# Kernel tuning notes

Measured on AMD Instinct MI355X. Metric: run time of the kernel, lower is better.

The kernel has to match this reference:

```python
import jax, jax.numpy as jnp
import numpy as np

B, C, H, W = 8, 256, 64, 64
D = C // 8  # query/key channels


def setup_inputs() -> dict:
    key = jax.random.key(0)
    ks = jax.random.split(key, 7)
    s = 0.05
    x = jax.random.normal(ks[0], (B, C, H, W), dtype=jnp.float32)
    Wq = jax.random.normal(ks[1], (D, C), dtype=jnp.float32) * s
    bq = jax.random.normal(ks[2], (D,), dtype=jnp.float32) * s
    Wk = jax.random.normal(ks[3], (D, C), dtype=jnp.float32) * s
    bk = jax.random.normal(ks[4], (D,), dtype=jnp.float32) * s
    Wv = jax.random.normal(ks[5], (C, C), dtype=jnp.float32) * s
    bv = jax.random.normal(ks[6], (C,), dtype=jnp.float32) * s
    return {"x": x, "Wq": Wq, "bq": bq, "Wk": Wk, "bk": bk, "Wv": Wv, "bv": bv}


def reference(x, Wq, bq, Wk, bk, Wv, bv):
    b, c, h, w = x.shape
    n = h * w
    xf = x.reshape(b, c, n)  # (B, C, HW)
    # 1x1 convs == per-pixel linear projections
    q = jnp.einsum('dc,bcn->bdn', Wq, xf) + bq[None, :, None]  # (B, D, HW)
    k = jnp.einsum('dc,bcn->bdn', Wk, xf) + bk[None, :, None]  # (B, D, HW)
    v = jnp.einsum('ec,bcn->ben', Wv, xf) + bv[None, :, None]  # (B, C, HW)
    # attention[b, n, m] = sum_d q[b,d,n] * k[b,d,m]  (no 1/sqrt(d) scaling)
    attn = jax.nn.softmax(jnp.einsum('bdn,bdm->bnm', q, k), axis=-1)
    # out[b,c,n] = sum_m v[b,c,m] * attn[b,n,m]  (v @ attn^T)
    out = jnp.einsum('bcm,bnm->bcn', v, attn)
    return out.reshape(b, c, h, w) + x
```

## Files before the change

kernel.cpp:

```cpp
#include <hip/hip_runtime.h>
#include <stdint.h>

#define BN 4096
#define NCH 256
#define DQ 32

typedef _Float16 half8  __attribute__((ext_vector_type(8)));
typedef _Float16 half4  __attribute__((ext_vector_type(4)));
typedef _Float16 half2  __attribute__((ext_vector_type(2)));
typedef float   floatx4  __attribute__((ext_vector_type(4)));
typedef float   floatx16 __attribute__((ext_vector_type(16)));

typedef __attribute__((address_space(1))) const void g1_void;
typedef __attribute__((address_space(3))) void l3_void;

#define LOG2E 1.44269504088896f
#define EXP2F(x) __builtin_amdgcn_exp2f(x)
#define LOG2F(x) __builtin_amdgcn_logf(x)

__global__ __launch_bounds__(256) void convert_w(
    const float* __restrict__ Wq, const float* __restrict__ Wk,
    const float* __restrict__ Wv, _Float16* __restrict__ W16)
{
    int e4 = (blockIdx.x * 256 + threadIdx.x) * 4;
    float4 v;
    if (e4 < 8192)        v = *(const float4*)&Wq[e4];
    else if (e4 < 16384) {
        v = *(const float4*)&Wk[e4 - 8192];
        v.x *= LOG2E; v.y *= LOG2E; v.z *= LOG2E; v.w *= LOG2E;
    }
    else                  v = *(const float4*)&Wv[e4 - 16384];
    half4 h = { (_Float16)v.x, (_Float16)v.y, (_Float16)v.z, (_Float16)v.w };
    *(half4*)&W16[e4] = h;
}

__global__ __launch_bounds__(512) void proj_kernel(
    const float* __restrict__ x, const _Float16* __restrict__ W16,
    const float* __restrict__ bq, const float* __restrict__ bk,
    const float* __restrict__ bv,
    _Float16* __restrict__ qT, _Float16* __restrict__ kT,
    _Float16* __restrict__ vb)
{
    const int t  = threadIdx.x;
    const int n0 = blockIdx.x * 128;
    const int b  = blockIdx.z;

    __shared__ __align__(16) _Float16 xTl[128 * 256];

#pragma unroll
    for (int p = 0; p < 2; ++p) {
        const int kb = p * 128 + (t >> 5) * 8;
        const int n4 = (t & 31) * 4;
        float4 xr[8];
#pragma unroll
        for (int i = 0; i < 8; ++i)
            xr[i] = *(const float4*)&x[((size_t)b * NCH + kb + i) * BN + n0 + n4];
        const float* xf = (const float*)xr;
#pragma unroll
        for (int j = 0; j < 4; ++j) {
            const int n = n4 + j;
            half8 hv;
#pragma unroll
            for (int i = 0; i < 8; ++i) hv[i] = (_Float16)xf[i * 4 + j];
            const int phys = (kb >> 3) ^ ((n >> 2) & 31);
            *(half8*)&xTl[n * 256 + phys * 8] = hv;
        }
    }
    __syncthreads();

    const int lane  = t & 63;
    const int gw    = blockIdx.y * 8 + (t >> 6);
    const int col32 = lane & 31;
    const int h     = lane >> 5;
    const int nc    = gw & 3;
    const int jj    = gw >> 2;

    const _Float16* Wq16 = W16;
    const _Float16* Wk16 = W16 + 8192;
    const _Float16* Wv16 = W16 + 16384;

#define XFRAG(ks) (*(const half8*)&xTl[(nc * 32 + col32) * 256 + \
        (((ks) * 2 + h) ^ (((nc * 32 + col32) >> 2) & 31)) * 8])

    if (jj == 0) {
        const float bqv = bq[col32];
        const float bkv = bk[col32] * LOG2E;
        floatx16 aq, ak2;
#pragma unroll
        for (int r = 0; r < 16; ++r) { aq[r] = 0.0f; ak2[r] = 0.0f; }
#pragma unroll
        for (int ks = 0; ks < 16; ++ks) {
            half8 xa = XFRAG(ks);
            half8 wqf = *(const half8*)&Wq16[col32 * 256 + ks * 16 + h * 8];
            half8 wkf = *(const half8*)&Wk16[col32 * 256 + ks * 16 + h * 8];
            aq  = __builtin_amdgcn_mfma_f32_32x32x16_f16(xa, wqf, aq, 0, 0, 0);
            ak2 = __builtin_amdgcn_mfma_f32_32x32x16_f16(xa, wkf, ak2, 0, 0, 0);
        }
#pragma unroll
        for (int r = 0; r < 16; ++r) {
            const int n = n0 + nc * 32 + (r & 3) + 8 * (r >> 2) + 4 * h;
            qT[((size_t)b * BN + n) * DQ + col32] = (_Float16)(aq[r] + bqv);
            kT[((size_t)b * BN + n) * DQ + col32] = (_Float16)(ak2[r] + bkv);
        }
    } else {
        const int rg_lo = (jj == 1) ? 0 : (jj == 2) ? 3 : 6;
        const int rg_hi = (jj == 1) ? 3 : (jj == 2) ? 6 : 8;
        for (int rg = rg_lo; rg < rg_hi; ++rg) {
            floatx16 av;
#pragma unroll
            for (int r = 0; r < 16; ++r) av[r] = 0.0f;
#pragma unroll
            for (int ks = 0; ks < 16; ++ks) {
                half8 xb  = XFRAG(ks);
                half8 wvf = *(const half8*)&Wv16[(rg * 32 + col32) * 256 + ks * 16 + h * 8];
                av = __builtin_amdgcn_mfma_f32_32x32x16_f16(wvf, xb, av, 0, 0, 0);
            }
#pragma unroll
            for (int r = 0; r < 16; ++r) {
                const int c = rg * 32 + (r & 3) + 8 * (r >> 2) + 4 * h;
                vb[((size_t)b * NCH + c) * BN + n0 + nc * 32 + col32] =
                    (_Float16)(av[r] + bv[c]);
            }
        }
    }
#undef XFRAG
}

__global__ __launch_bounds__(256, 3) void flash_kernel(
    const _Float16* __restrict__ qT, const _Float16* __restrict__ kT,
    const _Float16* __restrict__ vb,
    _Float16* __restrict__ Op, float* __restrict__ Ml, int KPS)
{
    const int t    = threadIdx.x;
    const int lane = t & 63;
    const int w    = t >> 6;
    const int n0   = blockIdx.x * 64;
    const int kh   = blockIdx.y;
    const int b    = blockIdx.z;
    const int kbase = kh * KPS;
    const int iters = (min(KPS, BN - kbase)) >> 6;

    __shared__ __align__(16) _Float16 vs[NCH * 64];
    __shared__ __align__(16) _Float16 Ps[2][64 * 64];
    __shared__ float alph_s[2][64];
    __shared__ float l_s[64];

    const int col   = lane & 15;
    const int q4    = lane >> 4;
    const int col32 = lane & 31;
    const int h     = lane >> 5;

    const _Float16* kp = kT + (size_t)b * BN * DQ;
    const _Float16* vp = vb + (size_t)b * NCH * BN;

    half8 bqf = *(const half8*)&qT[((size_t)b * BN + n0 + w * 16 + col) * DQ + q4 * 8];

    floatx16 acc[2][2];
#pragma unroll
    for (int ct = 0; ct < 2; ++ct)
#pragma unroll
        for (int nt = 0; nt < 2; ++nt)
#pragma unroll
            for (int r = 0; r < 16; ++r) acc[ct][nt][r] = 0.0f;

    float m_i = -1e30f, l_i = 0.0f;

    const int sc_loc = lane >> 3;
    const int s_log  = (lane & 7) ^ (sc_loc & 7);

    half8 ak[4];
    floatx4 sf[4];
    half4 pk[4];
    float al;

#define K_LOAD(MC)                                                          \
    do {                                                                    \
        _Pragma("unroll")                                                   \
        for (int mt = 0; mt < 4; ++mt)                                      \
            ak[mt] = *(const half8*)&kp[(size_t)((MC) + mt * 16 + col) * DQ + q4 * 8]; \
    } while (0)

#define V_DMA(MC)                                                           \
    do {                                                                    \
        _Pragma("unroll")                                                   \
        for (int j = 0; j < 8; ++j) {                                       \
            const int c = w * 64 + j * 8 + sc_loc;                          \
            __builtin_amdgcn_global_load_lds(                               \
                (g1_void*)&vp[(size_t)c * BN + (MC) + s_log * 8],           \
                (l3_void*)&vs[(w * 64 + j * 8) * 64], 16, 0, 0);            \
        }                                                                   \
    } while (0)

#define QK_STEP()                                                           \
    do {                                                                    \
        __builtin_amdgcn_s_setprio(1);                                      \
        _Pragma("unroll")                                                   \
        for (int mt = 0; mt < 4; ++mt) {                                    \
            floatx4 z = { 0.0f, 0.0f, 0.0f, 0.0f };                         \
            sf[mt] = __builtin_amdgcn_mfma_f32_16x16x32_f16(ak[mt], bqf, z, 0, 0, 0); \
        }                                                                   \
        __builtin_amdgcn_s_setprio(0);                                      \
    } while (0)

#define SM_STEP()                                                           \
    do {                                                                    \
        float cmax = -1e30f;                                                \
        _Pragma("unroll")                                                   \
        for (int mt = 0; mt < 4; ++mt)                                      \
            _Pragma("unroll")                                               \
            for (int r = 0; r < 4; ++r) cmax = fmaxf(cmax, sf[mt][r]);      \
        cmax = fmaxf(cmax, __shfl_xor(cmax, 16));                           \
        cmax = fmaxf(cmax, __shfl_xor(cmax, 32));                           \
        const float mn = (cmax > m_i + 8.0f) ? cmax : m_i;                  \
        al = EXP2F(m_i - mn);                                               \
        float csum = 0.0f;                                                  \
        _Pragma("unroll")                                                   \
        for (int mt = 0; mt < 4; ++mt) {                                    \
            float p0 = EXP2F(sf[mt][0] - mn);                               \
            float p1 = EXP2F(sf[mt][1] - mn);                               \
            float p2 = EXP2F(sf[mt][2] - mn);                               \
            float p3 = EXP2F(sf[mt][3] - mn);                               \
            csum += p0 + p1 + p2 + p3;                                      \
            half2 q01 = __builtin_bit_cast(half2, __builtin_amdgcn_cvt_pkrtz(p0, p1)); \
            half2 q23 = __builtin_bit_cast(half2, __builtin_amdgcn_cvt_pkrtz(p2, p3)); \
            pk[mt][0] = q01[0]; pk[mt][1] = q01[1];                         \
            pk[mt][2] = q23[0]; pk[mt][3] = q23[1];                         \
        }                                                                   \
        csum += __shfl_xor(csum, 16);                                       \
        csum += __shfl_xor(csum, 32);                                       \
        l_i = l_i * al + csum;                                              \
        m_i = mn;                                                           \
    } while (0)

#define PS_WRITE(BUF)                                                       \
    do {                                                                    \
        const int n = w * 16 + col;                                         \
        _Pragma("unroll")                                                   \
        for (int mt = 0; mt < 4; ++mt) {                                    \
            const int p_log = 2 * mt + (q4 >> 1);                           \
            const int p_phys = p_log ^ (n & 7);                             \
            *(half4*)((char*)&Ps[BUF][n * 64] + p_phys * 16 + (q4 & 1) * 8) = pk[mt]; \
        }                                                                   \
        if (q4 == 0) alph_s[BUF][n] = al;                                   \
    } while (0)

#define RESCALE(BUF)                                                        \
    do {                                                                    \
        float a0 = alph_s[BUF][col32];                                      \
        float a1 = alph_s[BUF][32 + col32];                                 \
        if (!__all((a0 == 1.0f) && (a1 == 1.0f))) {                         \
            _Pragma("unroll")                                               \
            for (int ct = 0; ct < 2; ++ct)                                  \
                _Pragma("unroll")                                           \
                for (int r = 0; r < 16; ++r) {                              \
                    acc[ct][0][r] *= a0;                                    \
                    acc[ct][1][r] *= a1;                                    \
                }                                                           \
        }                                                                   \
    } while (0)

#define PV_STEP(BUF)                                                        \
    do {                                                                    \
        __builtin_amdgcn_s_setprio(1);                                      \
        _Pragma("unroll")                                                   \
        for (int ks = 0; ks < 4; ++ks) {                                    \
            const int p_log = 2 * ks + h;                                   \
            half8 bp0 = *(const half8*)((char*)&Ps[BUF][col32 * 64] + (p_log ^ (col32 & 7)) * 16); \
            half8 bp1 = *(const half8*)((char*)&Ps[BUF][(32 + col32) * 64] + (p_log ^ (col32 & 7)) * 16); \
            _Pragma("unroll")                                               \
            for (int ct = 0; ct < 2; ++ct) {                                \
                const int c = w * 64 + ct * 32 + col32;                     \
                half8 av = *(const half8*)((char*)&vs[c * 64] + ((p_log ^ (c & 7)) * 16)); \
                acc[ct][0] = __builtin_amdgcn_mfma_f32_32x32x16_f16(av, bp0, acc[ct][0], 0, 0, 0); \
                acc[ct][1] = __builtin_amdgcn_mfma_f32_32x32x16_f16(av, bp1, acc[ct][1], 0, 0, 0); \
            }                                                               \
        }                                                                   \
        __builtin_amdgcn_s_setprio(0);                                      \
    } while (0)

    K_LOAD(kbase);
    V_DMA(kbase);
    QK_STEP();
    { const int m1 = (1 < iters) ? kbase + 64 : kbase; K_LOAD(m1); }
    SM_STEP();
    PS_WRITE(0);

    for (int it = 0; it < iters - 1; ++it) {
        const int cur = it & 1, nxt = cur ^ 1;
        asm volatile("s_waitcnt lgkmcnt(0)" ::: "memory");
        __builtin_amdgcn_s_barrier();
        QK_STEP();
        { const int m2 = (it + 2 < iters) ? kbase + (it + 2) * 64
                                          : kbase + (iters - 1) * 64;
          K_LOAD(m2); }
        RESCALE(cur);
        asm volatile("s_waitcnt vmcnt(4)" ::: "memory");
        PV_STEP(cur);
        SM_STEP();
        PS_WRITE(nxt);
        asm volatile("s_waitcnt lgkmcnt(0)" ::: "memory");
        V_DMA(kbase + (it + 1) * 64);
    }

    {
        const int cur = (iters - 1) & 1;
        asm volatile("s_waitcnt lgkmcnt(0)" ::: "memory");
        __builtin_amdgcn_s_barrier();
        RESCALE(cur);
        asm volatile("s_waitcnt vmcnt(0)" ::: "memory");
        PV_STEP(cur);
    }

    if (q4 == 0) {
        const int n = w * 16 + col;
        l_s[n] = l_i;
        Ml[(size_t)(kh * 8 + b) * BN + n0 + n] = m_i + LOG2F(l_i);
    }
    __syncthreads();
    const float li0 = 1.0f / l_s[col32];
    const float li1 = 1.0f / l_s[32 + col32];

    _Float16* Opp = Op + (size_t)(kh * 8 + b) * NCH * BN;
#pragma unroll
    for (int ct = 0; ct < 2; ++ct)
#pragma unroll
        for (int nt = 0; nt < 2; ++nt) {
            const float li = nt ? li1 : li0;
#pragma unroll
            for (int r = 0; r < 16; ++r) {
                int row = (r & 3) + 8 * (r >> 2) + 4 * h;
                int c = w * 64 + ct * 32 + row;
                Opp[(size_t)c * BN + n0 + nt * 32 + col32] = (_Float16)(acc[ct][nt][r] * li);
            }
        }
#undef K_LOAD
#undef V_DMA
#undef QK_STEP
#undef SM_STEP
#undef PS_WRITE
#undef RESCALE
#undef PV_STEP
}

__global__ __launch_bounds__(256) void combine_kernel(
    const _Float16* __restrict__ Op, const float* __restrict__ Ml,
    const float* __restrict__ x, float* __restrict__ out, int nsplit)
{
    const int n  = (blockIdx.x * 256 + threadIdx.x) * 8;
    const int c0 = blockIdx.y * 2;
    const int b  = blockIdx.z;

    float f[3][8];
    float Z[8];
#pragma unroll
    for (int j = 0; j < 8; ++j) Z[j] = -1e30f;
    for (int s = 0; s < nsplit; ++s) {
        const float* mlp = &Ml[(size_t)(s * 8 + b) * BN + n];
        floatx4 z0 = *(const floatx4*)mlp;
        floatx4 z1 = *(const floatx4*)(mlp + 4);
#pragma unroll
        for (int j = 0; j < 4; ++j) { f[s][j] = z0[j]; f[s][4 + j] = z1[j]; }
#pragma unroll
        for (int j = 0; j < 8; ++j) Z[j] = fmaxf(Z[j], f[s][j]);
    }
    float lsum[8];
#pragma unroll
    for (int j = 0; j < 8; ++j) lsum[j] = 0.0f;
    for (int s = 0; s < nsplit; ++s)
#pragma unroll
        for (int j = 0; j < 8; ++j) { f[s][j] = EXP2F(f[s][j] - Z[j]); lsum[j] += f[s][j]; }
#pragma unroll
    for (int j = 0; j < 8; ++j) lsum[j] = 1.0f / lsum[j];
    for (int s = 0; s < nsplit; ++s)
#pragma unroll
        for (int j = 0; j < 8; ++j) f[s][j] *= lsum[j];

#pragma unroll 2
    for (int ci = 0; ci < 2; ++ci) {
        const int c = c0 + ci;
        const size_t off = ((size_t)b * NCH + c) * BN + n;
        const size_t po = (size_t)c * BN + n;
        float ov[8];
#pragma unroll
        for (int j = 0; j < 8; ++j) ov[j] = 0.0f;
        for (int s = 0; s < nsplit; ++s) {
            half8 hv = *(const half8*)&Op[(size_t)(s * 8 + b) * NCH * BN + po];
#pragma unroll
            for (int j = 0; j < 8; ++j) ov[j] += (float)hv[j] * f[s][j];
        }
        floatx4 x0 = *(const floatx4*)&x[off];
        floatx4 x1 = *(const floatx4*)&x[off + 4];
        floatx4 o0, o1;
#pragma unroll
        for (int j = 0; j < 4; ++j) { o0[j] = ov[j] + x0[j]; o1[j] = ov[4 + j] + x1[j]; }
        *(floatx4*)&out[off] = o0;
        *(floatx4*)&out[off + 4] = o1;
    }
}

extern "C" void kernel_launch(void* const* d_in, const int* in_sizes, int n_in,
                              void* d_out, int out_size, void* d_ws, size_t ws_size,
                              hipStream_t stream)
{
    const float* x  = (const float*)d_in[0];
    const float* Wq = (const float*)d_in[1];
    const float* bq = (const float*)d_in[2];
    const float* Wk = (const float*)d_in[3];
    const float* bk = (const float*)d_in[4];
    const float* Wv = (const float*)d_in[5];
    const float* bv = (const float*)d_in[6];
    float* out = (float*)d_out;

    _Float16* ws = (_Float16*)d_ws;
    _Float16* W16 = ws;
    _Float16* qT  = W16 + 81920;
    _Float16* kT  = qT + (size_t)8 * BN * DQ;
    _Float16* vb  = kT + (size_t)8 * BN * DQ;
    _Float16* Op  = vb + (size_t)8 * NCH * BN;

    const size_t baseElems = 81920 + (size_t)2 * 8 * BN * DQ + (size_t)8 * NCH * BN;
    const size_t opElems3  = (size_t)3 * 8 * NCH * BN;
    const size_t mlBytes   = (size_t)24 * BN * sizeof(float);
    const size_t need3     = (baseElems + opElems3) * 2 + mlBytes + 256;
    const int nsplit = (ws_size >= need3) ? 3 : 2;
    const int KPS    = (nsplit == 3) ? 1408 : 2048;

    float* Ml = (float*)(Op + (size_t)nsplit * 8 * NCH * BN);

    convert_w<<<dim3(80), 256, 0, stream>>>(Wq, Wk, Wv, W16);
    proj_kernel<<<dim3(32, 2, 8), 512, 0, stream>>>(x, W16, bq, bk, bv, qT, kT, vb);
    flash_kernel<<<dim3(64, nsplit, 8), 256, 0, stream>>>(qT, kT, vb, Op, Ml, KPS);
    combine_kernel<<<dim3(2, 128, 8), 256, 0, stream>>>(Op, Ml, x, out, nsplit);
}
```

Before: 238.5 us.

## Warp-specialize flash kernel into QK/softmax producer and PV consumer waves

The flash attention block grows to 512 threads. Four waves now compute QK^T and the online softmax and write P and the rescale factors into double-buffered shared memory. The other four waves stream V into LDS and run the PV MFMAs with the accumulators, and the two groups stay in step through a shared barrier each iteration. The goal is to overlap the softmax work with the PV matrix work across waves. The cost is that V load latency is no longer hidden behind the K loads within a wave, and launch bounds of (512, 4) tighten the register budget per wave, which risks spills of the 64-float accumulator.

```diff
diff --git a/kernel.cpp b/kernel.cpp
--- a/kernel.cpp
+++ b/kernel.cpp
@@ -126,14 +126,14 @@
 #undef XFRAG
 }
 
-__global__ __launch_bounds__(256, 3) void flash_kernel(
+__global__ __launch_bounds__(512, 4) void flash_kernel(
     const _Float16* __restrict__ qT, const _Float16* __restrict__ kT,
     const _Float16* __restrict__ vb,
     _Float16* __restrict__ Op, float* __restrict__ Ml, int KPS)
 {
     const int t    = threadIdx.x;
     const int lane = t & 63;
-    const int w    = t >> 6;
+    const int wid  = t >> 6;
     const int n0   = blockIdx.x * 64;
     const int kh   = blockIdx.y;
     const int b    = blockIdx.z;
@@ -150,196 +150,194 @@
     const int col32 = lane & 31;
     const int h     = lane >> 5;
 
-    const _Float16* kp = kT + (size_t)b * BN * DQ;
-    const _Float16* vp = vb + (size_t)b * NCH * BN;
-
-    half8 bqf = *(const half8*)&qT[((size_t)b * BN + n0 + w * 16 + col) * DQ + q4 * 8];
-
-    floatx16 acc[2][2];
-#pragma unroll
-    for (int ct = 0; ct < 2; ++ct)
-#pragma unroll
-        for (int nt = 0; nt < 2; ++nt)
-#pragma unroll
-            for (int r = 0; r < 16; ++r) acc[ct][nt][r] = 0.0f;
-
-    float m_i = -1e30f, l_i = 0.0f;
-
-    const int sc_loc = lane >> 3;
-    const int s_log  = (lane & 7) ^ (sc_loc & 7);
-
-    half8 ak[4];
-    floatx4 sf[4];
-    half4 pk[4];
-    float al;
+    if (wid < 4) {
+        const int w = wid;
+        const _Float16* kp = kT + (size_t)b * BN * DQ;
+
+        half8 bqf = *(const half8*)&qT[((size_t)b * BN + n0 + w * 16 + col) * DQ + q4 * 8];
+        half8 ak[4];
+        floatx4 sf[4];
+        half4 pk[4];
+        float m_i = -1e30f, l_i = 0.0f, al = 1.0f;
 
 #define K_LOAD(MC)                                                          \
-    do {                                                                    \
-        _Pragma("unroll")                                                   \
-        for (int mt = 0; mt < 4; ++mt)                                      \
-            ak[mt] = *(const half8*)&kp[(size_t)((MC) + mt * 16 + col) * DQ + q4 * 8]; \
-    } while (0)
-
-#define V_DMA(MC)                                                           \
-    do {                                                                    \
-        _Pragma("unroll")                                                   \
-        for (int j = 0; j < 8; ++j) {                                       \
-            const int c = w * 64 + j * 8 + sc_loc;                          \
-            __builtin_amdgcn_global_load_lds(                               \
-                (g1_void*)&vp[(size_t)c * BN + (MC) + s_log * 8],           \
-                (l3_void*)&vs[(w * 64 + j * 8) * 64], 16, 0, 0);            \
-        }                                                                   \
-    } while (0)
+        do {                                                                \
+            _Pragma("unroll")                                               \
+            for (int mt = 0; mt < 4; ++mt)                                  \
+                ak[mt] = *(const half8*)&kp[(size_t)((MC) + mt * 16 + col) * DQ + q4 * 8]; \
+        } while (0)
 
 #define QK_STEP()                                                           \
-    do {                                                                    \
-        __builtin_amdgcn_s_setprio(1);                                      \
-        _Pragma("unroll")                                                   \
-        for (int mt = 0; mt < 4; ++mt) {                                    \
-            floatx4 z = { 0.0f, 0.0f, 0.0f, 0.0f };                         \
-            sf[mt] = __builtin_amdgcn_mfma_f32_16x16x32_f16(ak[mt], bqf, z, 0, 0, 0); \
-        }                                                                   \
-        __builtin_amdgcn_s_setprio(0);                                      \
-    } while (0)
+        do {                                                                \
+            __builtin_amdgcn_s_setprio(1);                                  \
+            _Pragma("unroll")                                               \
+            for (int mt = 0; mt < 4; ++mt) {                                \
+                floatx4 z = { 0.0f, 0.0f, 0.0f, 0.0f };                     \
+                sf[mt] = __builtin_amdgcn_mfma_f32_16x16x32_f16(ak[mt], bqf, z, 0, 0, 0); \
+            }                                                               \
+            __builtin_amdgcn_s_setprio(0);                                  \
+        } while (0)
 
 #define SM_STEP()                                                           \
-    do {                                                                    \
-        float cmax = -1e30f;                                                \
-        _Pragma("unroll")                                                   \
-        for (int mt = 0; mt < 4; ++mt)                                      \
-            _Pragma("unroll")                                               \
-            for (int r = 0; r < 4; ++r) cmax = fmaxf(cmax, sf[mt][r]);      \
-        cmax = fmaxf(cmax, __shfl_xor(cmax, 16));                           \
-        cmax = fmaxf(cmax, __shfl_xor(cmax, 32));                           \
-        const float mn = (cmax > m_i + 8.0f) ? cmax : m_i;                  \
-        al = EXP2F(m_i - mn);                                               \
-        float csum = 0.0f;                                                  \
-        _Pragma("unroll")                                                   \
-        for (int mt = 0; mt < 4; ++mt) {                                    \
-            float p0 = EXP2F(sf[mt][0] - mn);                               \
-            float p1 = EXP2F(sf[mt][1] - mn);                               \
-            float p2 = EXP2F(sf[mt][2] - mn);                               \
-            float p3 = EXP2F(sf[mt][3] - mn);                               \
-            csum += p0 + p1 + p2 + p3;                                      \
-            half2 q01 = __builtin_bit_cast(half2, __builtin_amdgcn_cvt_pkrtz(p0, p1)); \
-            half2 q23 = __builtin_bit_cast(half2, __builtin_amdgcn_cvt_pkrtz(p2, p3)); \
-            pk[mt][0] = q01[0]; pk[mt][1] = q01[1];                         \
-            pk[mt][2] = q23[0]; pk[mt][3] = q23[1];                         \
-        }                                                                   \
-        csum += __shfl_xor(csum, 16);                                       \
-        csum += __shfl_xor(csum, 32);                                       \
-        l_i = l_i * al + csum;                                              \
-        m_i = mn;                                                           \
-    } while (0)
+        do {                                                                \
+            float cmax = -1e30f;                                            \
+            _Pragma("unroll")                                               \
+            for (int mt = 0; mt < 4; ++mt)                                  \
+                _Pragma("unroll")                                           \
+                for (int r = 0; r < 4; ++r) cmax = fmaxf(cmax, sf[mt][r]);  \
+            cmax = fmaxf(cmax, __shfl_xor(cmax, 16));                       \
+            cmax = fmaxf(cmax, __shfl_xor(cmax, 32));                       \
+            const float mn = (cmax > m_i + 8.0f) ? cmax : m_i;              \
+            al = EXP2F(m_i - mn);                                           \
+            float csum = 0.0f;                                              \
+            _Pragma("unroll")                                               \
+            for (int mt = 0; mt < 4; ++mt) {                                \
+                float p0 = EXP2F(sf[mt][0] - mn);                           \
+                float p1 = EXP2F(sf[mt][1] - mn);                           \
+                float p2 = EXP2F(sf[mt][2] - mn);                           \
+                float p3 = EXP2F(sf[mt][3] - mn);                           \
+                csum += p0 + p1 + p2 + p3;                                  \
+                half2 q01 = __builtin_bit_cast(half2, __builtin_amdgcn_cvt_pkrtz(p0, p1)); \
+                half2 q23 = __builtin_bit_cast(half2, __builtin_amdgcn_cvt_pkrtz(p2, p3)); \
+                pk[mt][0] = q01[0]; pk[mt][1] = q01[1];                     \
+                pk[mt][2] = q23[0]; pk[mt][3] = q23[1];                     \
+            }                                                               \
+            csum += __shfl_xor(csum, 16);                                   \
+            csum += __shfl_xor(csum, 32);                                   \
+            l_i = l_i * al + csum;                                          \
+            m_i = mn;                                                       \
+        } while (0)
 
 #define PS_WRITE(BUF)                                                       \
-    do {                                                                    \
-        const int n = w * 16 + col;                                         \
-        _Pragma("unroll")                                                   \
-        for (int mt = 0; mt < 4; ++mt) {                                    \
-            const int p_log = 2 * mt + (q4 >> 1);                           \
-            const int p_phys = p_log ^ (n & 7);                             \
-            *(half4*)((char*)&Ps[BUF][n * 64] + p_phys * 16 + (q4 & 1) * 8) = pk[mt]; \
-        }                                                                   \
-        if (q4 == 0) alph_s[BUF][n] = al;                                   \
-    } while (0)
-
-#define RESCALE(BUF)                                                        \
-    do {                                                                    \
-        float a0 = alph_s[BUF][col32];                                      \
-        float a1 = alph_s[BUF][32 + col32];                                 \
-        if (!__all((a0 == 1.0f) && (a1 == 1.0f))) {                         \
-            _Pragma("unroll")                                               \
-            for (int ct = 0; ct < 2; ++ct)                                  \
-                _Pragma("unroll")                                           \
-                for (int r = 0; r < 16; ++r) {                              \
-                    acc[ct][0][r] *= a0;                                    \
-                    acc[ct][1][r] *= a1;                                    \
-                }                                                           \
-        }                                                                   \
-    } while (0)
-
-#define PV_STEP(BUF)                                                        \
-    do {                                                                    \
-        __builtin_amdgcn_s_setprio(1);                                      \
-        _Pragma("unroll")                                                   \
-        for (int ks = 0; ks < 4; ++ks) {                                    \
-            const int p_log = 2 * ks + h;                                   \
-            half8 bp0 = *(const half8*)((char*)&Ps[BUF][col32 * 64] + (p_log ^ (col32 & 7)) * 16); \
-            half8 bp1 = *(const half8*)((char*)&Ps[BUF][(32 + col32) * 64] + (p_log ^ (col32 & 7)) * 16); \
-            _Pragma("unroll")                                               \
-            for (int ct = 0; ct < 2; ++ct) {                                \
-                const int c = w * 64 + ct * 32 + col32;                     \
-                half8 av = *(const half8*)((char*)&vs[c * 64] + ((p_log ^ (c & 7)) * 16)); \
-                acc[ct][0] = __builtin_amdgcn_mfma_f32_32x32x16_f16(av, bp0, acc[ct][0], 0, 0, 0); \
-                acc[ct][1] = __builtin_amdgcn_mfma_f32_32x32x16_f16(av, bp1, acc[ct][1], 0, 0, 0); \
+        do {                                                                \
+            const int n = w * 16 + col;                                     \
+            _Pragma("unroll")                                               \
+            for (int mt = 0; mt < 4; ++mt) {                                \
+                const int p_log = 2 * mt + (q4 >> 1);                       \
+                const int p_phys = p_log ^ (n & 7);                         \
+                *(half4*)((char*)&Ps[BUF][n * 64] + p_phys * 16 + (q4 & 1) * 8) = pk[mt]; \
             }                                                               \
-        }                                                                   \
-        __builtin_amdgcn_s_setprio(0);                                      \
-    } while (0)
-
-    K_LOAD(kbase);
-    V_DMA(kbase);
-    QK_STEP();
-    { const int m1 = (1 < iters) ? kbase + 64 : kbase; K_LOAD(m1); }
-    SM_STEP();
-    PS_WRITE(0);
-
-    for (int it = 0; it < iters - 1; ++it) {
-        const int cur = it & 1, nxt = cur ^ 1;
-        asm volatile("s_waitcnt lgkmcnt(0)" ::: "memory");
-        __builtin_amdgcn_s_barrier();
+            if (q4 == 0) alph_s[BUF][n] = al;                               \
+        } while (0)
+
+        K_LOAD(kbase);
         QK_STEP();
-        { const int m2 = (it + 2 < iters) ? kbase + (it + 2) * 64
-                                          : kbase + (iters - 1) * 64;
-          K_LOAD(m2); }
-        RESCALE(cur);
-        asm volatile("s_waitcnt vmcnt(4)" ::: "memory");
-        PV_STEP(cur);
+        { const int m1 = (1 < iters) ? kbase + 64 : kbase; K_LOAD(m1); }
         SM_STEP();
-        PS_WRITE(nxt);
-        asm volatile("s_waitcnt lgkmcnt(0)" ::: "memory");
-        V_DMA(kbase + (it + 1) * 64);
-    }
-
-    {
-        const int cur = (iters - 1) & 1;
-        asm volatile("s_waitcnt lgkmcnt(0)" ::: "memory");
-        __builtin_amdgcn_s_barrier();
-        RESCALE(cur);
-        asm volatile("s_waitcnt vmcnt(0)" ::: "memory");
-        PV_STEP(cur);
-    }
-
-    if (q4 == 0) {
-        const int n = w * 16 + col;
-        l_s[n] = l_i;
-        Ml[(size_t)(kh * 8 + b) * BN + n0 + n] = m_i + LOG2F(l_i);
-    }
-    __syncthreads();
-    const float li0 = 1.0f / l_s[col32];
-    const float li1 = 1.0f / l_s[32 + col32];
-
-    _Float16* Opp = Op + (size_t)(kh * 8 + b) * NCH * BN;
-#pragma unroll
-    for (int ct = 0; ct < 2; ++ct)
-#pragma unroll
-        for (int nt = 0; nt < 2; ++nt) {
-            const float li = nt ? li1 : li0;
-#pragma unroll
-            for (int r = 0; r < 16; ++r) {
-                int row = (r & 3) + 8 * (r >> 2) + 4 * h;
-                int c = w * 64 + ct * 32 + row;
-                Opp[(size_t)c * BN + n0 + nt * 32 + col32] = (_Float16)(acc[ct][nt][r] * li);
-            }
+        PS_WRITE(0);
+
+        for (int it = 0; it < iters; ++it) {
+            asm volatile("s_waitcnt lgkmcnt(0)" ::: "memory");
+            __builtin_amdgcn_s_barrier();
+            if (it + 1 < iters) {
+                QK_STEP();
+                { const int m2 = (it + 2 < iters) ? kbase + (it + 2) * 64
+                                                  : kbase + (iters - 1) * 64;
+                  K_LOAD(m2); }
+                SM_STEP();
+                PS_WRITE((it + 1) & 1);
+            }
+        }
+
+        if (q4 == 0) {
+            const int n = w * 16 + col;
+            l_s[n] = l_i;
+            Ml[(size_t)(kh * 8 + b) * BN + n0 + n] = m_i + LOG2F(l_i);
         }
 #undef K_LOAD
-#undef V_DMA
 #undef QK_STEP
 #undef SM_STEP
 #undef PS_WRITE
-#undef RESCALE
-#undef PV_STEP
+    } else {
+        const int w = wid - 4;
+        const _Float16* vp = vb + (size_t)b * NCH * BN;
+        const int sc_loc = lane >> 3;
+        const int s_log  = (lane & 7) ^ (sc_loc & 7);
+
+        floatx16 acc[2][2];
+#pragma unroll
+        for (int ct = 0; ct < 2; ++ct)
+#pragma unroll
+            for (int nt = 0; nt < 2; ++nt)
+#pragma unroll
+                for (int r = 0; r < 16; ++r) acc[ct][nt][r] = 0.0f;
+
+#define V_DMA(MC)                                                           \
+        do {                                                                \
+            _Pragma("unroll")                                               \
+            for (int j = 0; j < 8; ++j) {                                   \
+                const int c = w * 64 + j * 8 + sc_loc;                      \
+                __builtin_amdgcn_global_load_lds(                           \
+                    (g1_void*)&vp[(size_t)c * BN + (MC) + s_log * 8],       \
+                    (l3_void*)&vs[(w * 64 + j * 8) * 64], 16, 0, 0);        \
+            }                                                               \
+        } while (0)
+
+        V_DMA(kbase);
+
+        for (int it = 0; it < iters; ++it) {
+            const int cur = it & 1;
+            asm volatile("s_waitcnt lgkmcnt(0)" ::: "memory");
+            __builtin_amdgcn_s_barrier();
+
+            {
+                float a0 = alph_s[cur][col32];
+                float a1 = alph_s[cur][32 + col32];
+                if (!__all((a0 == 1.0f) && (a1 == 1.0f))) {
+#pragma unroll
+                    for (int ct = 0; ct < 2; ++ct)
+#pragma unroll
+                        for (int r = 0; r < 16; ++r) {
+                            acc[ct][0][r] *= a0;
+                            acc[ct][1][r] *= a1;
+                        }
+                }
+            }
+
+            asm volatile("s_waitcnt vmcnt(0)" ::: "memory");
+
+            __builtin_amdgcn_s_setprio(1);
+#pragma unroll
+            for (int ks = 0; ks < 4; ++ks) {
+                const int p_log = 2 * ks + h;
+                half8 bp0 = *(const half8*)((char*)&Ps[cur][col32 * 64] + (p_log ^ (col32 & 7)) * 16);
+                half8 bp1 = *(const half8*)((char*)&Ps[cur][(32 + col32) * 64] + (p_log ^ (col32 & 7)) * 16);
+#pragma unroll
+                for (int ct = 0; ct < 2; ++ct) {
+                    const int c = w * 64 + ct * 32 + col32;
+                    half8 av = *(const half8*)((char*)&vs[c * 64] + ((p_log ^ (c & 7)) * 16));
+                    acc[ct][0] = __builtin_amdgcn_mfma_f32_32x32x16_f16(av, bp0, acc[ct][0], 0, 0, 0);
+                    acc[ct][1] = __builtin_amdgcn_mfma_f32_32x32x16_f16(av, bp1, acc[ct][1], 0, 0, 0);
+                }
+            }
+            __builtin_amdgcn_s_setprio(0);
+
+            if (it + 1 < iters) {
+                asm volatile("s_waitcnt lgkmcnt(0)" ::: "memory");
+                V_DMA(kbase + (it + 1) * 64);
+            }
+        }
+#undef V_DMA
+
+        __syncthreads();
+        const float li0 = 1.0f / l_s[col32];
+        const float li1 = 1.0f / l_s[32 + col32];
+        _Float16* Opp = Op + (size_t)(kh * 8 + b) * NCH * BN;
+#pragma unroll
+        for (int ct = 0; ct < 2; ++ct)
+#pragma unroll
+            for (int nt = 0; nt < 2; ++nt) {
+                const float li = nt ? li1 : li0;
+#pragma unroll
+                for (int r = 0; r < 16; ++r) {
+                    int row = (r & 3) + 8 * (r >> 2) + 4 * h;
+                    int c = w * 64 + ct * 32 + row;
+                    Opp[(size_t)c * BN + n0 + nt * 32 + col32] = (_Float16)(acc[ct][nt][r] * li);
+                }
+            }
+        return;
+    }
+    __syncthreads();
 }
 
 __global__ __launch_bounds__(256) void combine_kernel(
@@ -429,6 +427,6 @@
 
     convert_w<<<dim3(80), 256, 0, stream>>>(Wq, Wk, Wv, W16);
     proj_kernel<<<dim3(32, 2, 8), 512, 0, stream>>>(x, W16, bq, bk, bv, qT, kT, vb);
-    flash_kernel<<<dim3(64, nsplit, 8), 256, 0, stream>>>(qT, kT, vb, Op, Ml, KPS);
+    flash_kernel<<<dim3(64, nsplit, 8), 512, 0, stream>>>(qT, kT, vb, Op, Ml, KPS);
     combine_kernel<<<dim3(2, 128, 8), 256, 0, stream>>>(Op, Ml, x, out, nsplit);
 }
```

Result: no change. 238.1 us (-0.1%).

## Load V operands directly from global into registers instead of staging through LDS

Applied to the files above, without the earlier changes.

Removes the 32KB shared-memory V tile and its global_load_lds DMA. Each wave now loads its own V MFMA A-operands straight from global memory into registers, split into two halves to overlap with rescale and PV compute. This frees LDS, which could raise occupancy, and removes the LDS reads for V. In exchange the V loads are no longer prefetched an iteration ahead, so their latency is exposed within the same iteration, and register pressure goes up.

```diff
diff --git a/kernel.cpp b/kernel.cpp
--- a/kernel.cpp
+++ b/kernel.cpp
@@ -140,7 +140,6 @@
     const int kbase = kh * KPS;
     const int iters = (min(KPS, BN - kbase)) >> 6;
 
-    __shared__ __align__(16) _Float16 vs[NCH * 64];
     __shared__ __align__(16) _Float16 Ps[2][64 * 64];
     __shared__ float alph_s[2][64];
     __shared__ float l_s[64];
@@ -165,10 +164,8 @@
 
     float m_i = -1e30f, l_i = 0.0f;
 
-    const int sc_loc = lane >> 3;
-    const int s_log  = (lane & 7) ^ (sc_loc & 7);
-
     half8 ak[4];
+    half8 avA[2][2], avB[2][2];
     floatx4 sf[4];
     half4 pk[4];
     float al;
@@ -180,15 +177,15 @@
             ak[mt] = *(const half8*)&kp[(size_t)((MC) + mt * 16 + col) * DQ + q4 * 8]; \
     } while (0)
 
-#define V_DMA(MC)                                                           \
-    do {                                                                    \
-        _Pragma("unroll")                                                   \
-        for (int j = 0; j < 8; ++j) {                                       \
-            const int c = w * 64 + j * 8 + sc_loc;                          \
-            __builtin_amdgcn_global_load_lds(                               \
-                (g1_void*)&vp[(size_t)c * BN + (MC) + s_log * 8],           \
-                (l3_void*)&vs[(w * 64 + j * 8) * 64], 16, 0, 0);            \
-        }                                                                   \
+#define AV_LOAD(DST, MC, KS0)                                               \
+    do {                                                                    \
+        _Pragma("unroll")                                                   \
+        for (int kk = 0; kk < 2; ++kk)                                      \
+            _Pragma("unroll")                                               \
+            for (int ct = 0; ct < 2; ++ct) {                                \
+                const int c = w * 64 + ct * 32 + col32;                     \
+                DST[kk][ct] = *(const half8*)&vp[(size_t)c * BN + (MC) + (2 * ((KS0) + kk) + h) * 8]; \
+            }                                                               \
     } while (0)
 
 #define QK_STEP()                                                           \
@@ -259,27 +256,22 @@
         }                                                                   \
     } while (0)
 
-#define PV_STEP(BUF)                                                        \
-    do {                                                                    \
-        __builtin_amdgcn_s_setprio(1);                                      \
-        _Pragma("unroll")                                                   \
-        for (int ks = 0; ks < 4; ++ks) {                                    \
+#define PV_HALF(AV, BUF, KS0)                                               \
+    do {                                                                    \
+        _Pragma("unroll")                                                   \
+        for (int kk = 0; kk < 2; ++kk) {                                    \
+            const int ks = (KS0) + kk;                                      \
             const int p_log = 2 * ks + h;                                   \
             half8 bp0 = *(const half8*)((char*)&Ps[BUF][col32 * 64] + (p_log ^ (col32 & 7)) * 16); \
             half8 bp1 = *(const half8*)((char*)&Ps[BUF][(32 + col32) * 64] + (p_log ^ (col32 & 7)) * 16); \
-            _Pragma("unroll")                                               \
-            for (int ct = 0; ct < 2; ++ct) {                                \
-                const int c = w * 64 + ct * 32 + col32;                     \
-                half8 av = *(const half8*)((char*)&vs[c * 64] + ((p_log ^ (c & 7)) * 16)); \
-                acc[ct][0] = __builtin_amdgcn_mfma_f32_32x32x16_f16(av, bp0, acc[ct][0], 0, 0, 0); \
-                acc[ct][1] = __builtin_amdgcn_mfma_f32_32x32x16_f16(av, bp1, acc[ct][1], 0, 0, 0); \
-            }                                                               \
+            acc[0][0] = __builtin_amdgcn_mfma_f32_32x32x16_f16(AV[kk][0], bp0, acc[0][0], 0, 0, 0); \
+            acc[0][1] = __builtin_amdgcn_mfma_f32_32x32x16_f16(AV[kk][0], bp1, acc[0][1], 0, 0, 0); \
+            acc[1][0] = __builtin_amdgcn_mfma_f32_32x32x16_f16(AV[kk][1], bp0, acc[1][0], 0, 0, 0); \
+            acc[1][1] = __builtin_amdgcn_mfma_f32_32x32x16_f16(AV[kk][1], bp1, acc[1][1], 0, 0, 0); \
         }                                                                   \
-        __builtin_amdgcn_s_setprio(0);                                      \
     } while (0)
 
     K_LOAD(kbase);
-    V_DMA(kbase);
     QK_STEP();
     { const int m1 = (1 < iters) ? kbase + 64 : kbase; K_LOAD(m1); }
     SM_STEP();
@@ -287,28 +279,36 @@
 
     for (int it = 0; it < iters - 1; ++it) {
         const int cur = it & 1, nxt = cur ^ 1;
+        const int mc = kbase + it * 64;
         asm volatile("s_waitcnt lgkmcnt(0)" ::: "memory");
         __builtin_amdgcn_s_barrier();
         QK_STEP();
         { const int m2 = (it + 2 < iters) ? kbase + (it + 2) * 64
                                           : kbase + (iters - 1) * 64;
           K_LOAD(m2); }
+        AV_LOAD(avA, mc, 0);
         RESCALE(cur);
-        asm volatile("s_waitcnt vmcnt(4)" ::: "memory");
-        PV_STEP(cur);
+        AV_LOAD(avB, mc, 2);
+        __builtin_amdgcn_s_setprio(1);
+        PV_HALF(avA, cur, 0);
+        PV_HALF(avB, cur, 2);
+        __builtin_amdgcn_s_setprio(0);
         SM_STEP();
         PS_WRITE(nxt);
-        asm volatile("s_waitcnt lgkmcnt(0)" ::: "memory");
-        V_DMA(kbase + (it + 1) * 64);
     }
 
     {
         const int cur = (iters - 1) & 1;
+        const int mc = kbase + (iters - 1) * 64;
         asm volatile("s_waitcnt lgkmcnt(0)" ::: "memory");
         __builtin_amdgcn_s_barrier();
+        AV_LOAD(avA, mc, 0);
         RESCALE(cur);
-        asm volatile("s_waitcnt vmcnt(0)" ::: "memory");
-        PV_STEP(cur);
+        AV_LOAD(avB, mc, 2);
+        __builtin_amdgcn_s_setprio(1);
+        PV_HALF(avA, cur, 0);
+        PV_HALF(avB, cur, 2);
+        __builtin_amdgcn_s_setprio(0);
     }
 
     if (q4 == 0) {
@@ -334,12 +334,12 @@
             }
         }
 #undef K_LOAD
-#undef V_DMA
+#undef AV_LOAD
 #undef QK_STEP
 #undef SM_STEP
 #undef PS_WRITE
 #undef RESCALE
-#undef PV_STEP
+#undef PV_HALF
 }
 
 __global__ __launch_bounds__(256) void combine_kernel(
```

Result: slower. 292.0 us (+22.4%).
